# Performance work log

Hardware: AMD Instinct MI355X
Metric: run time of the kernel (lower is better)

Reference implementation:

```python
import jax, jax.numpy as jnp
import numpy as np

N_EMBD = 2048
DIM_ATT = 2048
HEAD_SIZE = 64
N_HEAD = DIM_ATT // HEAD_SIZE
D_MIX = 32
D_DECAY = 64
N_LAYER = 24
LAYER_ID = 12
EPS = 1e-5 * 8.0 ** 2  # GroupNorm eps with head_size_divisor=8


def setup_inputs() -> dict:
    key = jax.random.key(0)
    ks = jax.random.split(key, 10)
    B, T, C = 4, 2048, N_EMBD
    r0 = LAYER_ID / (N_LAYER - 1)          # ratio_0_to_1
    r1 = 1.0 - LAYER_ID / N_LAYER          # ratio_1_to_almost0
    ddd = (np.arange(C, dtype=np.float64) / C)
    f32 = np.float32
    time_maa_x = (1.0 - ddd ** r1).astype(f32)[None, None, :]
    time_maa_w = (1.0 - ddd ** r1).astype(f32)[None, None, :]
    time_maa_k = (1.0 - ddd ** r1).astype(f32)[None, None, :]
    time_maa_v = (1.0 - (ddd ** r1 + 0.3 * r0)).astype(f32)[None, None, :]
    time_maa_r = (1.0 - ddd ** (0.5 * r1)).astype(f32)[None, None, :]
    time_maa_g = (1.0 - ddd ** (0.5 * r1)).astype(f32)[None, None, :]
    n = np.arange(DIM_ATT, dtype=np.float64)
    decay_speed = (-6.0 + 5.0 * (n / (DIM_ATT - 1)) ** (0.7 + 1.3 * r0)).astype(f32)
    time_decay = decay_speed[None, None, :]
    zig = ((n + 1) % 3 - 1) * 0.1
    time_faaaa = (r0 * (1.0 - n / (DIM_ATT - 1)) + zig).astype(f32).reshape(N_HEAD, HEAD_SIZE)
    u = lambda k, sh: jax.random.uniform(k, sh, jnp.float32, -0.01, 0.01)
    inp = {
        'x': jax.random.normal(ks[0], (B, T, C), jnp.float32),
        'time_maa_x': jnp.asarray(time_maa_x), 'time_maa_w': jnp.asarray(time_maa_w),
        'time_maa_k': jnp.asarray(time_maa_k), 'time_maa_v': jnp.asarray(time_maa_v),
        'time_maa_r': jnp.asarray(time_maa_r), 'time_maa_g': jnp.asarray(time_maa_g),
        'time_maa_w1': u(ks[1], (C, D_MIX * 5)),
        'time_maa_w2': u(ks[2], (5, D_MIX, C)),
        'time_decay': jnp.asarray(time_decay),
        'time_decay_w1': u(ks[3], (C, D_DECAY)),
        'time_decay_w2': u(ks[4], (D_DECAY, DIM_ATT)),
        'time_faaaa': jnp.asarray(time_faaaa),
        'W_r': jax.random.normal(ks[5], (DIM_ATT, C), jnp.float32) * 0.02,
        'W_k': jax.random.normal(ks[6], (DIM_ATT, C), jnp.float32) * 0.02,
        'W_v': jax.random.normal(ks[7], (DIM_ATT, C), jnp.float32) * 0.02,
        'W_g': jax.random.normal(ks[8], (DIM_ATT, C), jnp.float32) * 0.02,
        'W_o': jax.random.normal(ks[9], (C, DIM_ATT), jnp.float32) * 0.02,
        'ln_gamma': jnp.ones((DIM_ATT,), jnp.float32),
        'ln_beta': jnp.zeros((DIM_ATT,), jnp.float32),
    }
    return inp


def _wkv6(r, k, v, w, u):
    # r,k,v,w: (B,T,H,N); u: (H,N). decay = exp(-exp(w)) applied per key-dim j.
    B, T, H, N = r.shape
    decay = jnp.exp(-jnp.exp(w))

    def step(S, inp):  # S: (B,H,N,N) indexed [b,h,j,i]
        r_t, k_t, v_t, d_t = inp  # each (B,H,N)
        kv = k_t[..., :, None] * v_t[..., None, :]          # (B,H,N,N)
        y = jnp.einsum('bhj,bhji->bhi', r_t, S + u[None, :, :, None] * kv)
        return d_t[..., None] * S + kv, y

    seq = (r.transpose(1, 0, 2, 3), k.transpose(1, 0, 2, 3),
           v.transpose(1, 0, 2, 3), decay.transpose(1, 0, 2, 3))
    S0 = jnp.zeros((B, H, N, N), r.dtype)
    _, ys = jax.lax.scan(step, S0, seq)                      # (T,B,H,N)
    return ys.transpose(1, 0, 2, 3)                          # (B,T,H,N)


def reference(x, time_maa_x, time_maa_w, time_maa_k, time_maa_v, time_maa_r, time_maa_g,
              time_maa_w1, time_maa_w2, time_decay, time_decay_w1, time_decay_w2,
              time_faaaa, W_r, W_k, W_v, W_g, W_o, ln_gamma, ln_beta):
    B, T, C = x.shape
    H, N = time_faaaa.shape
    xx = jnp.concatenate([jnp.zeros_like(x[:, :1]), x[:, :-1]], axis=1) - x  # time_shift - x
    xxx = x + xx * time_maa_x
    D = time_maa_w2.shape[1]
    a = jnp.tanh(xxx @ time_maa_w1).reshape(B, T, 5, D)
    m = jnp.einsum('btfd,fdc->fbtc', a, time_maa_w2)
    mw, mk, mv, mr, mg = m[0], m[1], m[2], m[3], m[4]
    xw = x + xx * (time_maa_w + mw)
    xk = x + xx * (time_maa_k + mk)
    xv = x + xx * (time_maa_v + mv)
    xr = x + xx * (time_maa_r + mr)
    xg = x + xx * (time_maa_g + mg)
    r = xr @ W_r.T
    k = xk @ W_k.T
    v = xv @ W_v.T
    g = jax.nn.silu(xg @ W_g.T)
    w = time_decay + jnp.tanh(xw @ time_decay_w1) @ time_decay_w2
    y = _wkv6(r.reshape(B, T, H, N), k.reshape(B, T, H, N),
              v.reshape(B, T, H, N), w.reshape(B, T, H, N), time_faaaa)
    # GroupNorm with H groups over channel dim
    mean = y.mean(-1, keepdims=True)
    var = y.var(-1, keepdims=True)
    yn = ((y - mean) * jax.lax.rsqrt(var + EPS)).reshape(B, T, H * N)
    yn = yn * ln_gamma + ln_beta
    return (yn * g) @ W_o.T
```

## Files before the change

### kernel.cpp

```cpp
#include <hip/hip_runtime.h>
#include <hip/hip_bf16.h>
#include <math.h>

#define B_ 4
#define T_ 2048
#define C_ 2048
#define H_ 32
#define BT_ 8192
#define WELE 4194304L
#define BTC  16777216L
#define NCH_ 16
#define TC_  128
#define GNT  32

typedef unsigned short u16;
typedef __bf16 bf16x8 __attribute__((ext_vector_type(8)));
typedef float  f32x4  __attribute__((ext_vector_type(4)));

__device__ __forceinline__ u16 f2b(float f){
  __hip_bfloat16 h = __float2bfloat16(f);
  return *reinterpret_cast<u16*>(&h);
}
__device__ __forceinline__ float b2f(u16 u){
  __hip_bfloat16 h; *reinterpret_cast<u16*>(&h) = u;
  return __bfloat162float(h);
}
__device__ __forceinline__ float bits2f(unsigned u){
  union { unsigned u; float f; } c; c.u = u; return c.f;
}

__device__ __forceinline__ void async_copy16(const u16* gptr, u16* lptr){
  __builtin_amdgcn_global_load_lds(
      (const __attribute__((address_space(1))) unsigned int*)gptr,
      (__attribute__((address_space(3))) unsigned int*)lptr,
      16, 0, 0);
}

__device__ __forceinline__ void unpack4(const u16* __restrict__ gp, float* out){
  const uint2 raw = *(const uint2*)gp;
  out[0] = bits2f(raw.x << 16); out[1] = bits2f(raw.x & 0xffff0000u);
  out[2] = bits2f(raw.y << 16); out[3] = bits2f(raw.y & 0xffff0000u);
}

__global__ __launch_bounds__(256) void cvt1(const float* __restrict__ src,
                                            u16* __restrict__ dst)
{
  const long i = ((long)blockIdx.x*256 + threadIdx.x)*4;
  const float4 v = *(const float4*)(src + i);
  ushort4 o = { f2b(v.x), f2b(v.y), f2b(v.z), f2b(v.w) };
  *(ushort4*)(dst + i) = o;
}

__global__ __launch_bounds__(256) void tposeA(const float* __restrict__ src,
    u16* __restrict__ dst, int R, int Cc, int Npad)
{
  const long idx = (long)blockIdx.x*256 + threadIdx.x;
  if (idx >= (long)Npad * R) return;
  const int n = (int)(idx / R), rr = (int)(idx % R);
  float vv = (n < Cc) ? src[(long)rr * Cc + n] : 0.f;
  dst[idx] = f2b(vv);
}

__global__ __launch_bounds__(256) void tposeW2(const float* __restrict__ src,
                                               u16* __restrict__ dst)
{
  const long idx = (long)blockIdx.x*256 + threadIdx.x;
  const int f = (int)(idx / 65536);
  const int rem = (int)(idx % 65536);
  const int c = rem >> 5, d = rem & 31;
  dst[idx] = f2b(src[((long)f*32 + d)*2048 + c]);
}

__global__ __launch_bounds__(256) void mixA(const float* __restrict__ x,
    const float* __restrict__ maax, u16* __restrict__ xxx, u16* __restrict__ xxb,
    u16* __restrict__ xbf)
{
  const long i = ((long)blockIdx.x*256 + threadIdx.x) * 4;
  const int c   = (int)(i & (C_-1));
  const int tok = (int)(i >> 11);
  const int t   = tok & (T_-1);
  const float4 xc = *(const float4*)(x + i);
  float4 xp = make_float4(0.f,0.f,0.f,0.f);
  if (t > 0) xp = *(const float4*)(x + i - C_);
  const float4 mx = *(const float4*)(maax + c);
  const float xx0 = xp.x - xc.x, xx1 = xp.y - xc.y;
  const float xx2 = xp.z - xc.z, xx3 = xp.w - xc.w;
  ushort4 ox = { f2b(xx0), f2b(xx1), f2b(xx2), f2b(xx3) };
  ushort4 o3 = { f2b(fmaf(xx0, mx.x, xc.x)), f2b(fmaf(xx1, mx.y, xc.y)),
                 f2b(fmaf(xx2, mx.z, xc.z)), f2b(fmaf(xx3, mx.w, xc.w)) };
  ushort4 oxb = { f2b(xc.x), f2b(xc.y), f2b(xc.z), f2b(xc.w) };
  *(ushort4*)(xxb + i) = ox;
  *(ushort4*)(xxx + i) = o3;
  *(ushort4*)(xbf + i) = oxb;
}

enum { EPI_BF16=0, EPI_TANH=1, EPI_SILU=2, EPI_MIX=3, EPI_DECAY=4, EPI_F32=5 };

template<int EPI>
__global__ __launch_bounds__(256) void gemm_bt(
    const u16* __restrict__ A, int lda,
    const u16* __restrict__ Bm, int ldb, int K,
    void* __restrict__ Out, int ldo,
    const float* __restrict__ aux0, const u16* __restrict__ aux1,
    const float* __restrict__ aux2)
{
  __shared__ u16 As[128*32];
  __shared__ u16 Bs[128*32];
  const int tid = threadIdx.x;
  const int w = tid >> 6, lane = tid & 63;
  const int m0 = blockIdx.y * 128, n0 = blockIdx.x * 128;
  const int wm = w >> 1, wn = w & 1;
  const int rowA = lane >> 2, chunk = lane & 3;
  f32x4 acc[4][4];
  #pragma unroll
  for (int i=0;i<4;i++)
    #pragma unroll
    for (int j=0;j<4;j++) acc[i][j] = (f32x4){0.f,0.f,0.f,0.f};

  for (int k0 = 0; k0 < K; k0 += 32){
    #pragma unroll
    for (int s=0; s<2; s++){
      const int seg = w*2 + s;
      const int row = seg*16 + rowA;
      async_copy16(A  + (long)(m0+row)*lda + k0 + chunk*8, As + seg*512);
      async_copy16(Bm + (long)(n0+row)*ldb + k0 + chunk*8, Bs + seg*512);
    }
    __syncthreads();
    const int kq = (lane >> 4) * 8;
    const int lr16 = lane & 15;
    bf16x8 af[4], bfr[4];
    #pragma unroll
    for (int mt=0; mt<4; mt++)
      af[mt] = *(const bf16x8*)(As + (wm*64 + mt*16 + lr16)*32 + kq);
    #pragma unroll
    for (int nt=0; nt<4; nt++)
      bfr[nt] = *(const bf16x8*)(Bs + (wn*64 + nt*16 + lr16)*32 + kq);
    #pragma unroll
    for (int mt=0; mt<4; mt++)
      #pragma unroll
      for (int nt=0; nt<4; nt++)
        acc[mt][nt] = __builtin_amdgcn_mfma_f32_16x16x32_bf16(af[mt], bfr[nt], acc[mt][nt], 0, 0, 0);
    __syncthreads();
  }

  const int cr = lane & 15, cq = lane >> 4;
  #pragma unroll
  for (int mt=0; mt<4; mt++){
    #pragma unroll
    for (int nt=0; nt<4; nt++){
      #pragma unroll
      for (int rr=0; rr<4; rr++){
        const int row = m0 + wm*64 + mt*16 + cq*4 + rr;
        const int col = n0 + wn*64 + nt*16 + cr;
        const long oi = (long)row*ldo + col;
        const float val = acc[mt][nt][rr];
        if constexpr (EPI == EPI_F32){
          ((float*)Out)[oi] = val;
        } else if constexpr (EPI == EPI_BF16){
          ((u16*)Out)[oi] = f2b(val);
        } else if constexpr (EPI == EPI_TANH){
          ((u16*)Out)[oi] = f2b(tanhf(val));
        } else if constexpr (EPI == EPI_SILU){
          ((u16*)Out)[oi] = f2b(val / (1.f + expf(-val)));
        } else if constexpr (EPI == EPI_MIX){
          const float xv  = b2f(((const u16*)aux0)[oi]);
          const float xxv = b2f(aux1[oi]);
          ((u16*)Out)[oi] = f2b(fmaf(xxv, aux2[col] + val, xv));
        } else {
          ((float*)Out)[oi] = expf(-expf(val + aux0[col]));
        }
      }
    }
  }
}

template<int EPI>
__global__ __launch_bounds__(512) void gemm256(
    const u16* __restrict__ A, const u16* __restrict__ Bm,
    void* __restrict__ Out, int ldo)
{
  __shared__ u16 lds[65536];
  const int tid  = threadIdx.x;
  const int w    = tid >> 6, lane = tid & 63;
  const int wm   = w >> 2, wn = w & 3;
  const long m0  = (long)blockIdx.y * 256;
  const long n0  = (long)blockIdx.x * 256;

  auto stage_half = [&](u16* ldsbase, const u16* gb){
    const int rsub = lane >> 3;
    const int c16  = (lane & 7) ^ rsub;
    #pragma unroll
    for (int r2 = 0; r2 < 2; ++r2){
      const int row = (r2*8 + w)*8 + rsub;
      async_copy16(gb + (long)row*2048 + c16*8,
                   ldsbase + (r2*8 + w)*512);
    }
  };
  auto stage = [&](int t, int half){
    if (t >= GNT) return;
    const int b = t & 1;
    const long k0 = (long)t * 64;
    if      (half == 0) stage_half(lds + 32768 + b*16384,        Bm + n0*2048 + k0);
    else if (half == 1) stage_half(lds + 32768 + b*16384 + 8192, Bm + (n0+128)*2048 + k0);
    else if (half == 2) stage_half(lds + b*16384,                A  + m0*2048 + k0);
    else                stage_half(lds + b*16384 + 8192,         A  + (m0+128)*2048 + k0);
  };

  const int lr16 = lane & 15;
  const int kq   = lane >> 4;
  auto aslot = [&](int buf, int row, int c16)->const u16*{
    return lds + buf*16384 + row*64 + ((c16 ^ (row & 7)) << 3);
  };
  auto bslot = [&](int buf, int row, int c16)->const u16*{
    return lds + 32768 + buf*16384 + row*64 + ((c16 ^ (row & 7)) << 3);
  };

  f32x4 acc[8][4];
  #pragma unroll
  for (int i=0;i<8;i++)
    #pragma unroll
    for (int j=0;j<4;j++) acc[i][j] = (f32x4){0.f,0.f,0.f,0.f};

  stage(0,0); stage(0,1); stage(0,2); stage(0,3);
  stage(1,0); stage(1,1); stage(1,2);
  asm volatile("s_waitcnt vmcnt(6)");
  asm volatile("" ::: "memory");
  __builtin_amdgcn_s_barrier();

  for (int t = 0; t < GNT; ++t){
    const int buf = t & 1;
    bf16x8 bfr[4][2];
    #pragma unroll
    for (int p = 0; p < 4; ++p){
      if (p == 0){
        #pragma unroll
        for (int nt=0; nt<4; nt++)
          #pragma unroll
          for (int kk=0; kk<2; kk++)
            bfr[nt][kk] = *(const bf16x8*)bslot(buf, wn*64 + nt*16 + lr16, kk*4 + kq);
      }
      bf16x8 af[2][2];
      #pragma unroll
      for (int i=0; i<2; i++)
        #pragma unroll
        for (int kk=0; kk<2; kk++)
          af[i][kk] = *(const bf16x8*)aslot(buf, wm*128 + (2*p+i)*16 + lr16, kk*4 + kq);
      if (p == 0) stage(t+1, 3);
      else        stage(t+2, p-1);
      if (p == 3){
        if (t <= GNT-3) asm volatile("s_waitcnt vmcnt(6)");
        else            asm volatile("s_waitcnt vmcnt(0)");
      }
      asm volatile("" ::: "memory");
      __builtin_amdgcn_s_barrier();
      __builtin_amdgcn_s_setprio(1);
      #pragma unroll
      for (int i=0; i<2; i++)
        #pragma unroll
        for (int nt=0; nt<4; nt++)
          #pragma unroll
          for (int kk=0; kk<2; kk++)
            acc[2*p+i][nt] = __builtin_amdgcn_mfma_f32_16x16x32_bf16(
                af[i][kk], bfr[nt][kk], acc[2*p+i][nt], 0, 0, 0);
      __builtin_amdgcn_s_setprio(0);
    }
  }

  const int cr = lane & 15, cq = lane >> 4;
  #pragma unroll
  for (int mt=0; mt<8; mt++){
    #pragma unroll
    for (int nt=0; nt<4; nt++){
      #pragma unroll
      for (int rr=0; rr<4; rr++){
        const long row = m0 + wm*128 + mt*16 + cq*4 + rr;
        const long col = n0 + wn*64 + nt*16 + cr;
        const long oi  = row*ldo + col;
        const float val = acc[mt][nt][rr];
        if constexpr (EPI == EPI_F32){
          ((float*)Out)[oi] = val;
        } else if constexpr (EPI == EPI_BF16){
          ((u16*)Out)[oi] = f2b(val);
        } else {
          ((u16*)Out)[oi] = f2b(val / (1.f + expf(-val)));
        }
      }
    }
  }
}


__global__ __launch_bounds__(256) void wkv_pass1(
    const u16* __restrict__ k, const u16* __restrict__ v,
    const float* __restrict__ dec,
    float* __restrict__ Sbuf, float* __restrict__ Dbuf)
{
  const int blk = blockIdx.x;
  const int c  = blk & (NCH_-1);
  if (c == NCH_-1) return;
  const int bh = blk >> 4;
  const int b = bh >> 5, h = bh & 31;
  const int tid = threadIdx.x;
  const int g = tid >> 6, lane = tid & 63;
  const int hoff = h * 64;
  const long base0 = ((long)b * T_) * C_ + hoff;
  const int tA = c * TC_;

  __shared__ float kts[128][64];
  __shared__ u16   vsh[128][64];
  __shared__ float Gp[4][64];

  #pragma unroll
  for (int rd = 0; rd < 4; ++rd){
    const int row0 = (rd*4 + g) * 8;
    async_copy16(v + base0 + (long)(tA + row0 + (lane>>3))*C_ + (lane&7)*8,
                 &vsh[row0][0]);
  }

  float d[32];
  float gp = 1.f;
  #pragma unroll
  for (int tau = 0; tau < 32; ++tau){
    d[tau] = dec[base0 + (long)(tA + g*32 + tau)*C_ + lane];
    gp *= d[tau];
  }
  Gp[g][lane] = gp;
  __syncthreads();
  float CS = 1.f;
  #pragma unroll
  for (int gg = 0; gg < 4; ++gg)
    if (gg > g) CS *= Gp[gg][lane];
  if (g == 0){
    Dbuf[(long)blk*64 + lane] =
        Gp[0][lane]*Gp[1][lane]*Gp[2][lane]*Gp[3][lane];
  }
  {
    float R = CS;
    #pragma unroll
    for (int tau = 31; tau >= 0; --tau){
      const float kv = b2f(k[base0 + (long)(tA + g*32 + tau)*C_ + lane]);
      kts[g*32 + tau][lane] = kv * R;
      R *= d[tau];
    }
  }
  __syncthreads();

  const int joff = g * 16;
  float S[16];
  #pragma unroll
  for (int jj=0;jj<16;jj++) S[jj]=0.f;
  #pragma unroll 4
  for (int t = 0; t < TC_; ++t){
    float kv[16];
    #pragma unroll
    for (int q=0;q<4;q++)
      *(float4*)(kv+q*4) = *(const float4*)&kts[t][joff+q*4];
    const float vi = b2f(vsh[t][lane]);
    #pragma unroll
    for (int jj=0;jj<16;jj++)
      S[jj] = fmaf(kv[jj], vi, S[jj]);
  }
  float* Sp = Sbuf + (long)blk*4096 + (long)joff*64 + lane;
  #pragma unroll
  for (int jj=0;jj<16;jj++) Sp[jj*64] = S[jj];
}

__global__ __launch_bounds__(256) void wkv_pass2(
    float* __restrict__ Sbuf, const float* __restrict__ Dbuf)
{
  const int bh = blockIdx.x >> 4;
  const int f  = ((blockIdx.x & 15) << 8) + threadIdx.x;
  const int j = f >> 6;
  float cur = 0.f;
  const long sbase = (long)bh * NCH_ * 4096 + f;
  const long dbase = (long)bh * NCH_ * 64 + j;
  for (int c = 0; c < NCH_-1; c++){
    float* Sp = Sbuf + sbase + (long)c*4096;
    const float tmp = *Sp;
    *Sp = cur;
    cur = fmaf(Dbuf[dbase + (long)c*64], cur, tmp);
  }
  Sbuf[sbase + (long)(NCH_-1)*4096] = cur;
}

__global__ __launch_bounds__(256) void wkv_pass3(
    const u16* __restrict__ r, const u16* __restrict__ k, const u16* __restrict__ v,
    const float* __restrict__ dec, const float* __restrict__ faaaa,
    const float* __restrict__ gam, const float* __restrict__ bet,
    const u16* __restrict__ g, u16* __restrict__ act,
    const float* __restrict__ Sbuf)
{
  const int blk = blockIdx.x;
  const int c  = blk & (NCH_-1);
  const int bh = blk >> 4;
  const int b = bh >> 5, h = bh & 31;
  const int tid = threadIdx.x;
  const int wv = tid >> 6, lane = tid & 63;
  const int hoff = h * 64;
  const int joff = wv * 16;

  float W[16];
  {
    const float* Sp = Sbuf + (long)blk*4096 + (long)joff*64 + lane;
    #pragma unroll
    for (int jj=0;jj<16;jj++) W[jj] = Sp[jj*64];
  }
  const float uu  = faaaa[hoff + lane];
  const float gmv = gam[hoff + lane], btv = bet[hoff + lane];

  __shared__ float rhat[32][64];
  __shared__ float ktil[32][64];
  __shared__ u16   vsh[32][64];
  __shared__ float yred[16][4][64];
  __shared__ float Gp[4][64];
  __shared__ float cendL[64];
  __shared__ float ud[32];

  const long base0 = ((long)b * T_) * C_ + hoff;
  const int tA = c * TC_;

  for (int sc = 0; sc < TC_/32; ++sc){
    const int t0 = tA + sc*32;
    __syncthreads();
    async_copy16(v + base0 + (long)(t0 + wv*8 + (lane>>3))*C_ + (lane&7)*8,
                 &vsh[wv*8][0]);
    float dloc[8];
    float gp = 1.f;
    #pragma unroll
    for (int tau=0; tau<8; ++tau){
      dloc[tau] = dec[base0 + (long)(t0 + wv*8 + tau)*C_ + lane];
      gp *= dloc[tau];
    }
    Gp[wv][lane] = gp;
    __syncthreads();
    float cpre = 1.f;
    #pragma unroll
    for (int gg=0; gg<4; ++gg) if (gg < wv) cpre *= Gp[gg][lane];
    if (wv == 0)
      cendL[lane] = Gp[0][lane]*Gp[1][lane]*Gp[2][lane]*Gp[3][lane];
    {
      float cc = cpre;
      #pragma unroll
      for (int tau=0; tau<8; ++tau){
        const int tl = wv*8 + tau;
        const long gi = base0 + (long)(t0 + tl)*C_ + lane;
        const float rv = b2f(r[gi]);
        const float kv = b2f(k[gi]);
        rhat[tl][lane] = rv * cc;
        float z = rv * uu * kv;
        cc *= dloc[tau];
        ktil[tl][lane] = kv / cc;
        #pragma unroll
        for (int off=32; off>0; off>>=1) z += __shfl_xor(z, off, 64);
        if (lane == 0) ud[tl] = z;
      }
    }
    __syncthreads();

    #pragma unroll
    for (int half=0; half<2; ++half){
      #pragma unroll 2
      for (int tt=0; tt<16; ++tt){
        const int tl = half*16 + tt;
        float rv[16], kt[16];
        #pragma unroll
        for (int q=0;q<4;q++){
          *(float4*)(rv+q*4) = *(const float4*)&rhat[tl][joff+q*4];
          *(float4*)(kt+q*4) = *(const float4*)&ktil[tl][joff+q*4];
        }
        const float vi = b2f(vsh[tl][lane]);
        float yp = 0.f;
        #pragma unroll
        for (int jj=0;jj<16;jj++){
          yp = fmaf(rv[jj], W[jj], yp);
          W[jj] = fmaf(kt[jj], vi, W[jj]);
        }
        yred[tt][wv][lane] = yp;
      }
      __syncthreads();
      #pragma unroll
      for (int q=0;q<4;q++){
        const int tt = wv*4 + q;
        const int tl = half*16 + tt;
        const float y = yred[tt][0][lane] + yred[tt][1][lane]
                      + yred[tt][2][lane] + yred[tt][3][lane]
                      + ud[tl] * b2f(vsh[tl][lane]);
        float s1 = y, s2 = y*y;
        #pragma unroll
        for (int off=32; off>0; off>>=1){
          s1 += __shfl_xor(s1, off, 64);
          s2 += __shfl_xor(s2, off, 64);
        }
        const float mean = s1 * (1.f/64.f);
        const float var  = s2 * (1.f/64.f) - mean*mean;
        const float yn   = (y - mean) * rsqrtf(var + 6.4e-4f);
        const long  oi   = base0 + (long)(t0 + tl) * C_ + lane;
        const float o    = (yn * gmv + btv) * b2f(g[oi]);
        act[oi] = f2b(o);
      }
      if (half == 0) __syncthreads();
    }
    #pragma unroll
    for (int jj=0;jj<16;jj++) W[jj] *= cendL[joff + jj];
  }
}

extern "C" void kernel_launch(void* const* d_in, const int* in_sizes, int n_in,
                              void* d_out, int out_size, void* d_ws, size_t ws_size,
                              hipStream_t stream)
{
  const float* x     = (const float*)d_in[0];
  const float* tmx   = (const float*)d_in[1];
  const float* maaf[5] = {(const float*)d_in[2], (const float*)d_in[3],
                          (const float*)d_in[4], (const float*)d_in[5],
                          (const float*)d_in[6]};
  const float* w1    = (const float*)d_in[7];
  const float* w2    = (const float*)d_in[8];
  const float* td    = (const float*)d_in[9];
  const float* tdw1  = (const float*)d_in[10];
  const float* tdw2  = (const float*)d_in[11];
  const float* faaaa = (const float*)d_in[12];
  const float* Wmat[5] = {(const float*)d_in[13], (const float*)d_in[14],
                          (const float*)d_in[15], (const float*)d_in[16],
                          (const float*)d_in[17]};
  const float* ln_g  = (const float*)d_in[18];
  const float* ln_b  = (const float*)d_in[19];

  char* p = (char*)d_ws;
  auto take = [&](size_t bytes)->char*{
    char* q = p; p += (bytes + 255) & ~(size_t)255; return q;
  };
  u16*   w1t  = (u16*)take(256L*2048*2);
  u16*   w2t  = (u16*)take(5L*2048*32*2);
  u16*   wd1t = (u16*)take(128L*2048*2);
  u16*   wd2t = (u16*)take(2048L*64*2);
  u16*   wcur = (u16*)take(WELE*2);
  u16*   xxx  = (u16*)take(BTC*2);
  u16*   xxb  = (u16*)take(BTC*2);
  u16*   abuf = (u16*)take((long)BT_*256*2);
  u16*   hbuf = (u16*)take((long)BT_*128*2);
  u16*   kbuf = (u16*)take(BTC*2);
  u16*   vbuf = (u16*)take(BTC*2);
  u16*   gbuf = (u16*)take(BTC*2);
  u16*   mixbuf = xxx;
  u16*   rbuf   = xxb;
  u16*   act    = kbuf;
  float* dcy    = (float*)d_out;
  u16*   xbf    = (u16*)d_out;
  float* Sbuf   = (float*)mixbuf;
  float* Dbuf   = (float*)hbuf;
  (void)in_sizes; (void)n_in; (void)out_size; (void)ws_size;

  tposeA <<<2048, 256, 0, stream>>>(w1,   w1t,  2048, 160, 256);
  tposeW2<<<1280, 256, 0, stream>>>(w2,   w2t);
  tposeA <<<1024, 256, 0, stream>>>(tdw1, wd1t, 2048, 64, 128);
  tposeA <<<512,  256, 0, stream>>>(tdw2, wd2t, 64, 2048, 2048);

  mixA<<<16384, 256, 0, stream>>>(x, tmx, xxx, xxb, xbf);

  gemm_bt<EPI_TANH><<<dim3(2,64), 256, 0, stream>>>(xxx, 2048, w1t, 2048, 2048,
      abuf, 256, nullptr, nullptr, nullptr);

  gemm_bt<EPI_MIX><<<dim3(16,64), 256, 0, stream>>>(abuf + 1*32, 256,
      w2t + 1L*65536, 32, 32, mixbuf, 2048, (const float*)xbf, xxb, maaf[1]);
  cvt1<<<4096, 256, 0, stream>>>(Wmat[1], wcur);
  gemm256<EPI_BF16><<<dim3(8,32), 512, 0, stream>>>(mixbuf, wcur, kbuf, 2048);

  gemm_bt<EPI_MIX><<<dim3(16,64), 256, 0, stream>>>(abuf + 2*32, 256,
      w2t + 2L*65536, 32, 32, mixbuf, 2048, (const float*)xbf, xxb, maaf[2]);
  cvt1<<<4096, 256, 0, stream>>>(Wmat[2], wcur);
  gemm256<EPI_BF16><<<dim3(8,32), 512, 0, stream>>>(mixbuf, wcur, vbuf, 2048);

  gemm_bt<EPI_MIX><<<dim3(16,64), 256, 0, stream>>>(abuf + 4*32, 256,
      w2t + 4L*65536, 32, 32, mixbuf, 2048, (const float*)xbf, xxb, maaf[4]);
  cvt1<<<4096, 256, 0, stream>>>(Wmat[3], wcur);
  gemm256<EPI_SILU><<<dim3(8,32), 512, 0, stream>>>(mixbuf, wcur, gbuf, 2048);

  gemm_bt<EPI_MIX><<<dim3(16,64), 256, 0, stream>>>(abuf + 0*32, 256,
      w2t + 0L*65536, 32, 32, mixbuf, 2048, (const float*)xbf, xxb, maaf[0]);
  gemm_bt<EPI_TANH><<<dim3(1,64), 256, 0, stream>>>(mixbuf, 2048, wd1t, 2048, 2048,
      hbuf, 128, nullptr, nullptr, nullptr);

  gemm_bt<EPI_MIX><<<dim3(16,64), 256, 0, stream>>>(abuf + 3*32, 256,
      w2t + 3L*65536, 32, 32, mixbuf, 2048, (const float*)xbf, xxb, maaf[3]);
  cvt1<<<4096, 256, 0, stream>>>(Wmat[0], wcur);
  gemm256<EPI_BF16><<<dim3(8,32), 512, 0, stream>>>(mixbuf, wcur, rbuf, 2048);

  gemm_bt<EPI_DECAY><<<dim3(16,64), 256, 0, stream>>>(hbuf, 128, wd2t, 64, 64,
      dcy, 2048, td, nullptr, nullptr);

  wkv_pass1<<<128*NCH_, 256, 0, stream>>>(kbuf, vbuf, dcy, Sbuf, Dbuf);
  wkv_pass2<<<128*NCH_, 256, 0, stream>>>(Sbuf, Dbuf);
  wkv_pass3<<<128*NCH_, 256, 0, stream>>>(rbuf, kbuf, vbuf, dcy, faaaa,
      ln_g, ln_b, gbuf, act, Sbuf);

  cvt1<<<4096, 256, 0, stream>>>(Wmat[4], wcur);
  gemm256<EPI_F32><<<dim3(8,32), 512, 0, stream>>>(act, wcur, d_out, 2048);
}
```

Before: 992.4 us.

## Recast chunked WKV pass3 as bf16 MFMA intra-chunk matmuls

Rewrites the per-chunk WKV pass from scalar per-timestep FMA recurrence into a chunked linear-attention form using 16x16x32 bf16 MFMA. Each chunk now computes r·S, a causally masked r·kᵀ matrix times v, and a kᵀv state update, with the state held in MFMA accumulators. GroupNorm reduction is restructured for the MFMA output layout. The aim is to remove the serial FMA loop over timesteps and use matrix cores. In exchange, the state, r-hat, k-tilde and attention matrix are rounded to bf16, and k/cc can become large, which risks accuracy loss.

```diff
diff --git a/kernel.cpp b/kernel.cpp
--- a/kernel.cpp
+++ b/kernel.cpp
@@ -395,61 +395,72 @@
   const int bh = blk >> 4;
   const int b = bh >> 5, h = bh & 31;
   const int tid = threadIdx.x;
-  const int wv = tid >> 6, lane = tid & 63;
+  const int w = tid >> 6, lane = tid & 63;
+  const int lr16 = lane & 15, hq = lane >> 4;
   const int hoff = h * 64;
-  const int joff = wv * 16;
-
-  float W[16];
-  {
-    const float* Sp = Sbuf + (long)blk*4096 + (long)joff*64 + lane;
-    #pragma unroll
-    for (int jj=0;jj<16;jj++) W[jj] = Sp[jj*64];
-  }
-  const float uu  = faaaa[hoff + lane];
-  const float gmv = gam[hoff + lane], btv = bet[hoff + lane];
-
-  __shared__ float rhat[32][64];
-  __shared__ float ktil[32][64];
-  __shared__ u16   vsh[32][64];
-  __shared__ float yred[16][4][64];
+  const long base0 = ((long)b * T_) * C_ + hoff;
+  const int tA = c * TC_;
+  const int iqs = w * 16;
+  const int mtM = w >> 1, ntM = w & 1;
+
+  __shared__ u16  rh_tj[32][72];
+  __shared__ u16  kt_tj[32][72];
+  __shared__ u16  ktT[64][40];
+  __shared__ u16  vT[64][40];
+  __shared__ u16  Whi[64][72];
+  __shared__ u16  Mld[32][40];
   __shared__ float Gp[4][64];
   __shared__ float cendL[64];
   __shared__ float ud[32];
-
-  const long base0 = ((long)b * T_) * C_ + hoff;
-  const int tA = c * TC_;
+  __shared__ float sr1[32][4], sr2[32][4];
+
+  f32x4 Wacc[4];
+  #pragma unroll
+  for (int jt=0;jt<4;jt++)
+    #pragma unroll
+    for (int rr=0;rr<4;rr++)
+      Wacc[jt][rr] = Sbuf[(long)blk*4096 + (long)(jt*16 + hq*4 + rr)*64 + iqs + lr16];
+
+  const float uu  = faaaa[hoff + lane];
+  const float gmv = gam[hoff + iqs + lr16];
+  const float btv = bet[hoff + iqs + lr16];
 
   for (int sc = 0; sc < TC_/32; ++sc){
     const int t0 = tA + sc*32;
-    __syncthreads();
-    async_copy16(v + base0 + (long)(t0 + wv*8 + (lane>>3))*C_ + (lane&7)*8,
-                 &vsh[wv*8][0]);
-    float dloc[8];
-    float gp = 1.f;
+    #pragma unroll
+    for (int jt=0; jt<4; ++jt){
+      const unsigned lo = (unsigned)f2b(Wacc[jt][0]) | ((unsigned)f2b(Wacc[jt][1]) << 16);
+      const unsigned hi = (unsigned)f2b(Wacc[jt][2]) | ((unsigned)f2b(Wacc[jt][3]) << 16);
+      *(uint2*)&Whi[iqs + lr16][jt*16 + hq*4] = make_uint2(lo, hi);
+    }
+    float dloc[8], gp = 1.f;
     #pragma unroll
     for (int tau=0; tau<8; ++tau){
-      dloc[tau] = dec[base0 + (long)(t0 + wv*8 + tau)*C_ + lane];
+      dloc[tau] = dec[base0 + (long)(t0 + w*8 + tau)*C_ + lane];
       gp *= dloc[tau];
     }
-    Gp[wv][lane] = gp;
+    Gp[w][lane] = gp;
     __syncthreads();
     float cpre = 1.f;
     #pragma unroll
-    for (int gg=0; gg<4; ++gg) if (gg < wv) cpre *= Gp[gg][lane];
-    if (wv == 0)
+    for (int gg=0; gg<4; ++gg) if (gg < w) cpre *= Gp[gg][lane];
+    if (w == 0)
       cendL[lane] = Gp[0][lane]*Gp[1][lane]*Gp[2][lane]*Gp[3][lane];
     {
       float cc = cpre;
       #pragma unroll
       for (int tau=0; tau<8; ++tau){
-        const int tl = wv*8 + tau;
+        const int tl = w*8 + tau;
         const long gi = base0 + (long)(t0 + tl)*C_ + lane;
         const float rv = b2f(r[gi]);
         const float kv = b2f(k[gi]);
-        rhat[tl][lane] = rv * cc;
+        rh_tj[tl][lane] = f2b(rv * cc);
         float z = rv * uu * kv;
         cc *= dloc[tau];
-        ktil[tl][lane] = kv / cc;
+        const u16 ktb = f2b(kv / cc);
+        kt_tj[tl][lane] = ktb;
+        ktT[lane][tl]   = ktb;
+        vT[lane][tl]    = v[gi];
         #pragma unroll
         for (int off=32; off>0; off>>=1) z += __shfl_xor(z, off, 64);
         if (lane == 0) ud[tl] = z;
@@ -457,51 +468,88 @@
     }
     __syncthreads();
 
-    #pragma unroll
-    for (int half=0; half<2; ++half){
-      #pragma unroll 2
-      for (int tt=0; tt<16; ++tt){
-        const int tl = half*16 + tt;
-        float rv[16], kt[16];
-        #pragma unroll
-        for (int q=0;q<4;q++){
-          *(float4*)(rv+q*4) = *(const float4*)&rhat[tl][joff+q*4];
-          *(float4*)(kt+q*4) = *(const float4*)&ktil[tl][joff+q*4];
-        }
-        const float vi = b2f(vsh[tl][lane]);
-        float yp = 0.f;
-        #pragma unroll
-        for (int jj=0;jj<16;jj++){
-          yp = fmaf(rv[jj], W[jj], yp);
-          W[jj] = fmaf(kt[jj], vi, W[jj]);
-        }
-        yred[tt][wv][lane] = yp;
-      }
-      __syncthreads();
-      #pragma unroll
-      for (int q=0;q<4;q++){
-        const int tt = wv*4 + q;
-        const int tl = half*16 + tt;
-        const float y = yred[tt][0][lane] + yred[tt][1][lane]
-                      + yred[tt][2][lane] + yred[tt][3][lane]
-                      + ud[tl] * b2f(vsh[tl][lane]);
+    f32x4 Yacc[2] = { (f32x4){0.f,0.f,0.f,0.f}, (f32x4){0.f,0.f,0.f,0.f} };
+    f32x4 Macc = (f32x4){0.f,0.f,0.f,0.f};
+    bf16x8 afR[2][2], bW[2], bK[2];
+    #pragma unroll
+    for (int mt=0; mt<2; ++mt)
+      #pragma unroll
+      for (int kh=0; kh<2; ++kh)
+        afR[mt][kh] = *(const bf16x8*)&rh_tj[mt*16 + lr16][kh*32 + hq*8];
+    #pragma unroll
+    for (int kh=0; kh<2; ++kh){
+      bW[kh] = *(const bf16x8*)&Whi[iqs + lr16][kh*32 + hq*8];
+      bK[kh] = *(const bf16x8*)&kt_tj[ntM*16 + lr16][kh*32 + hq*8];
+    }
+    #pragma unroll
+    for (int mt=0; mt<2; ++mt)
+      #pragma unroll
+      for (int kh=0; kh<2; ++kh)
+        Yacc[mt] = __builtin_amdgcn_mfma_f32_16x16x32_bf16(afR[mt][kh], bW[kh], Yacc[mt], 0,0,0);
+    #pragma unroll
+    for (int kh=0; kh<2; ++kh)
+      Macc = __builtin_amdgcn_mfma_f32_16x16x32_bf16(afR[mtM][kh], bK[kh], Macc, 0,0,0);
+    #pragma unroll
+    for (int rr=0; rr<4; ++rr){
+      const int tg = mtM*16 + hq*4 + rr;
+      const int sg = ntM*16 + lr16;
+      Mld[tg][sg] = f2b((sg < tg) ? Macc[rr] : 0.f);
+    }
+    __syncthreads();
+
+    bf16x8 aM[2], bV, aKT[4];
+    #pragma unroll
+    for (int mt=0; mt<2; ++mt)
+      aM[mt] = *(const bf16x8*)&Mld[mt*16 + lr16][hq*8];
+    bV = *(const bf16x8*)&vT[iqs + lr16][hq*8];
+    #pragma unroll
+    for (int jt=0; jt<4; ++jt)
+      aKT[jt] = *(const bf16x8*)&ktT[jt*16 + lr16][hq*8];
+    #pragma unroll
+    for (int mt=0; mt<2; ++mt)
+      Yacc[mt] = __builtin_amdgcn_mfma_f32_16x16x32_bf16(aM[mt], bV, Yacc[mt], 0,0,0);
+    #pragma unroll
+    for (int jt=0; jt<4; ++jt)
+      Wacc[jt] = __builtin_amdgcn_mfma_f32_16x16x32_bf16(aKT[jt], bV, Wacc[jt], 0,0,0);
+
+    #pragma unroll
+    for (int mt=0; mt<2; ++mt){
+      #pragma unroll
+      for (int rr=0; rr<4; ++rr){
+        const int tl = mt*16 + hq*4 + rr;
+        const float y = Yacc[mt][rr] + ud[tl] * b2f(vT[iqs + lr16][tl]);
+        Yacc[mt][rr] = y;
         float s1 = y, s2 = y*y;
         #pragma unroll
-        for (int off=32; off>0; off>>=1){
+        for (int off=1; off<16; off<<=1){
           s1 += __shfl_xor(s1, off, 64);
           s2 += __shfl_xor(s2, off, 64);
         }
-        const float mean = s1 * (1.f/64.f);
-        const float var  = s2 * (1.f/64.f) - mean*mean;
-        const float yn   = (y - mean) * rsqrtf(var + 6.4e-4f);
-        const long  oi   = base0 + (long)(t0 + tl) * C_ + lane;
-        const float o    = (yn * gmv + btv) * b2f(g[oi]);
-        act[oi] = f2b(o);
+        if (lr16 == 0){ sr1[tl][w] = s1; sr2[tl][w] = s2; }
       }
-      if (half == 0) __syncthreads();
-    }
-    #pragma unroll
-    for (int jj=0;jj<16;jj++) W[jj] *= cendL[joff + jj];
+    }
+    __syncthreads();
+    #pragma unroll
+    for (int mt=0; mt<2; ++mt){
+      #pragma unroll
+      for (int rr=0; rr<4; ++rr){
+        const int tl = mt*16 + hq*4 + rr;
+        const f32x4 a1 = *(const f32x4*)&sr1[tl][0];
+        const f32x4 a2 = *(const f32x4*)&sr2[tl][0];
+        const float S1 = a1[0]+a1[1]+a1[2]+a1[3];
+        const float S2 = a2[0]+a2[1]+a2[2]+a2[3];
+        const float mean = S1 * (1.f/64.f);
+        const float var  = S2 * (1.f/64.f) - mean*mean;
+        const float yn   = (Yacc[mt][rr] - mean) * rsqrtf(var + 6.4e-4f);
+        const long  oi   = base0 + (long)(t0 + tl)*C_ + iqs + lr16;
+        act[oi] = f2b((yn * gmv + btv) * b2f(g[oi]));
+      }
+    }
+    #pragma unroll
+    for (int jt=0; jt<4; ++jt)
+      #pragma unroll
+      for (int rr=0; rr<4; ++rr)
+        Wacc[jt][rr] *= cendL[jt*16 + hq*4 + rr];
   }
 }
 
```

Measured after the change: 1.161 ms. 17.0% more time.
